# Kernel tuning notes

Measured on AMD Instinct MI355X. Metric: run time of the kernel, lower is better.

Reference implementation:

```python
import jax, jax.numpy as jnp
import numpy as np

N_NODES = 50000
N_EDGES = 800000
IN_DIM = 128
OUT_DIM = 128


def setup_inputs() -> dict:
    key = jax.random.key(0)
    k_h, k_w, k_src, k_dst = jax.random.split(key, 4)
    h = jax.random.normal(k_h, (N_NODES, IN_DIM), dtype=jnp.float32)
    # xavier-uniform weight
    limit = float(np.sqrt(6.0 / (IN_DIM + OUT_DIM)))
    W = jax.random.uniform(k_w, (IN_DIM, OUT_DIM), dtype=jnp.float32,
                           minval=-limit, maxval=limit)
    b = jnp.zeros((OUT_DIM,), dtype=jnp.float32)
    src = jax.random.randint(k_src, (N_EDGES,), 0, N_NODES, dtype=jnp.int64)
    dst = jax.random.randint(k_dst, (N_EDGES,), 0, N_NODES, dtype=jnp.int64)
    # GCN symmetric norm: deg^{-1/2} based on in-degree (clamped to >=1)
    deg = jax.ops.segment_sum(jnp.ones((N_EDGES,), jnp.float32), dst,
                              num_segments=N_NODES)
    norm = (jnp.maximum(deg, 1.0) ** -0.5)[:, None]  # [N,1]
    return {"h": h, "norm": norm, "W": W, "b": b, "src": src, "dst": dst}


def reference(h, norm, W, b, src, dst):
    # dense projection: [N, in] @ [in, out]
    h = h @ W
    # pre-aggregation norm scale
    h = h * norm
    # copy_src + sum: gather source features, segment-sum into destination nodes
    msgs = h[src]  # [E, out]
    h = jax.ops.segment_sum(msgs, dst, num_segments=h.shape[0])
    # post-aggregation norm scale + bias
    h = h * norm + b
    return h
```

## Files before the change

kernel.cpp:

```cpp
#include <hip/hip_runtime.h>

#define N_NODES 50000
#define N_EDGES 800000

#define NBUCKETS 391
#define BIN_EDGES 4096
#define BIN_NB 196
#define BUCKET_CAP 2560

#define GEMM_NB ((N_NODES + 63) / 64)
#define FUSED_NB 980

typedef __attribute__((ext_vector_type(4))) _Float16 half4;
typedef __attribute__((ext_vector_type(8))) _Float16 half8;
typedef __attribute__((ext_vector_type(4))) float f32x4;

__global__ __launch_bounds__(256) void prep_wt_kernel(
    const float* __restrict__ W, _Float16* __restrict__ Wt)
{
    const int e = blockIdx.x * 256 + threadIdx.x;
    const int c = e & 127;
    const int k4 = (e >> 7) << 2;
    half4 v;
    v.x = (_Float16)W[(k4 + 0) * 128 + c];
    v.y = (_Float16)W[(k4 + 1) * 128 + c];
    v.z = (_Float16)W[(k4 + 2) * 128 + c];
    v.w = (_Float16)W[(k4 + 3) * 128 + c];
    *(half4*)(Wt + (size_t)c * 128 + k4) = v;
}

__global__ __launch_bounds__(256) void fused_gemm_bin_kernel(
    const float* __restrict__ h, const float* __restrict__ norm,
    const _Float16* __restrict__ Wt, _Float16* __restrict__ t,
    const int* __restrict__ src, const int* __restrict__ dst,
    int* __restrict__ bcur, int* __restrict__ bucketbuf)
{
    __shared__ int hist[NBUCKETS];
    __shared__ __align__(16) _Float16 WtS[128 * 136];
    const int tid = threadIdx.x;
    const int bid = blockIdx.x;

    if (bid % 5 == 4) {
        const int bs = (bid / 5) * BIN_EDGES;
        for (int i = tid; i < NBUCKETS; i += 256) hist[i] = 0;
        __syncthreads();
#pragma unroll
        for (int j = 0; j < 4; ++j) {
            int e4 = bs + (j * 256 + tid) * 4;
            if (e4 < N_EDGES) {
                int4 d4 = *(const int4*)(dst + e4);
                atomicAdd(&hist[d4.x >> 7], 1);
                atomicAdd(&hist[d4.y >> 7], 1);
                atomicAdd(&hist[d4.z >> 7], 1);
                atomicAdd(&hist[d4.w >> 7], 1);
            }
        }
        __syncthreads();
        for (int i = tid; i < NBUCKETS; i += 256) {
            int hc = hist[i];
            hist[i] = hc ? atomicAdd(&bcur[i], hc) : 0;
        }
        __syncthreads();
#pragma unroll
        for (int j = 0; j < 4; ++j) {
            int e4 = bs + (j * 256 + tid) * 4;
            if (e4 < N_EDGES) {
                int4 d4 = *(const int4*)(dst + e4);
                int4 s4 = *(const int4*)(src + e4);
                int b0, p;
                b0 = d4.x >> 7; p = atomicAdd(&hist[b0], 1);
                bucketbuf[(size_t)b0 * BUCKET_CAP + p] = s4.x | ((d4.x & 127) << 16);
                b0 = d4.y >> 7; p = atomicAdd(&hist[b0], 1);
                bucketbuf[(size_t)b0 * BUCKET_CAP + p] = s4.y | ((d4.y & 127) << 16);
                b0 = d4.z >> 7; p = atomicAdd(&hist[b0], 1);
                bucketbuf[(size_t)b0 * BUCKET_CAP + p] = s4.z | ((d4.z & 127) << 16);
                b0 = d4.w >> 7; p = atomicAdd(&hist[b0], 1);
                bucketbuf[(size_t)b0 * BUCKET_CAP + p] = s4.w | ((d4.w & 127) << 16);
            }
        }
        return;
    }

    const int gemm_id = bid - bid / 5;
    if (gemm_id >= GEMM_NB) return;
    const int rbase = gemm_id * 64;

#pragma unroll
    for (int i = 0; i < 8; ++i) {
        int f = i * 256 + tid;
        int c = f >> 4;
        int k8 = (f & 15) << 3;
        *(half8*)(WtS + c * 136 + k8) = *(const half8*)(Wt + (size_t)c * 128 + k8);
    }
    __syncthreads();

    const int wid = tid >> 6, lane = tid & 63;
    const int lrow = lane & 15;
    const int khi = (lane >> 4) << 3;
    const int r0 = wid * 16;
    const int gr = rbase + r0 + lrow;

    half8 a[4];
#pragma unroll
    for (int ks = 0; ks < 4; ++ks) {
        float4 f0 = make_float4(0.f, 0.f, 0.f, 0.f);
        float4 f1 = f0;
        if (gr < N_NODES) {
            const float* hp = h + (size_t)gr * 128 + ks * 32 + khi;
            f0 = *(const float4*)hp;
            f1 = *(const float4*)(hp + 4);
        }
        half8 av;
        av[0] = (_Float16)f0.x; av[1] = (_Float16)f0.y;
        av[2] = (_Float16)f0.z; av[3] = (_Float16)f0.w;
        av[4] = (_Float16)f1.x; av[5] = (_Float16)f1.y;
        av[6] = (_Float16)f1.z; av[7] = (_Float16)f1.w;
        a[ks] = av;
    }

    const int rq = rbase + r0 + ((lane >> 4) << 2);
    float nv[4];
#pragma unroll
    for (int reg = 0; reg < 4; ++reg)
        nv[reg] = (rq + reg < N_NODES) ? norm[rq + reg] : 0.f;

#pragma unroll
    for (int ct = 0; ct < 8; ++ct) {
        const int c0 = ct * 16;
        f32x4 acc = {0.f, 0.f, 0.f, 0.f};
#pragma unroll
        for (int ks = 0; ks < 4; ++ks) {
            half8 bf = *(const half8*)(WtS + (c0 + lrow) * 136 + ks * 32 + khi);
            acc = __builtin_amdgcn_mfma_f32_16x16x32_f16(a[ks], bf, acc, 0, 0, 0);
        }
#pragma unroll
        for (int reg = 0; reg < 4; ++reg) {
            if (rq + reg < N_NODES)
                t[(size_t)(rq + reg) * 128 + c0 + lrow] = (_Float16)(acc[reg] * nv[reg]);
        }
    }
}

__global__ __launch_bounds__(256) void scatter_kernel(
    const int* __restrict__ bucketbuf, const int* __restrict__ bcur,
    int* __restrict__ off, int* __restrict__ cur, int* __restrict__ esrc)
{
    const int tid = threadIdx.x;
    const int b = blockIdx.x;
    __shared__ int hist[128];
    __shared__ int lcur[128];
    if (tid < 128) hist[tid] = 0;
    __syncthreads();

    const int n = bcur[b];
    const int* buf = bucketbuf + (size_t)b * BUCKET_CAP;
    for (int i = tid; i < n; i += 256)
        atomicAdd(&hist[(buf[i] >> 16) & 127], 1);
    __syncthreads();

    const int cnt = (tid < 128) ? hist[tid] : 0;
    for (int d = 1; d < 128; d <<= 1) {
        int v = 0;
        if (tid < 128 && tid >= d) v = hist[tid - d];
        __syncthreads();
        if (tid < 128) hist[tid] += v;
        __syncthreads();
    }
    const int base = b * BUCKET_CAP;
    int o0 = 0;
    if (tid < 128) {
        o0 = base + hist[tid] - cnt;
        lcur[tid] = o0;
    }
    __syncthreads();
    for (int i = tid; i < n; i += 256) {
        int p = buf[i];
        int pos = atomicAdd(&lcur[(p >> 16) & 127], 1);
        esrc[pos] = p & 0xFFFF;
    }
    __syncthreads();
    const int g = b * 128 + tid;
    if (tid < 128 && g < N_NODES) {
        off[g] = o0;
        cur[g] = lcur[tid];
    }
}

__global__ __launch_bounds__(256) void aggregate_kernel(
    const int* __restrict__ off, const int* __restrict__ cur,
    const int* __restrict__ esrc, const _Float16* __restrict__ t,
    const float* __restrict__ norm, const float* __restrict__ b,
    float* __restrict__ out)
{
    const int g = blockIdx.x * 16 + (threadIdx.x >> 4);
    if (g >= N_NODES) return;
    const int l = threadIdx.x & 15;
    const int c = l << 3;
    const int i0 = off[g], i1 = cur[g];

    float acc0[8], acc1[8], acc2[8], acc3[8];
#pragma unroll
    for (int j = 0; j < 8; ++j) {
        acc0[j] = 0.f; acc1[j] = 0.f; acc2[j] = 0.f; acc3[j] = 0.f;
    }

    int i = i0;
    for (; i + 4 <= i1; i += 4) {
        int s0 = esrc[i], s1 = esrc[i + 1], s2 = esrc[i + 2], s3 = esrc[i + 3];
        half8 v0 = *(const half8*)(t + (size_t)s0 * 128 + c);
        half8 v1 = *(const half8*)(t + (size_t)s1 * 128 + c);
        half8 v2 = *(const half8*)(t + (size_t)s2 * 128 + c);
        half8 v3 = *(const half8*)(t + (size_t)s3 * 128 + c);
#pragma unroll
        for (int j = 0; j < 8; ++j) {
            acc0[j] += (float)v0[j]; acc1[j] += (float)v1[j];
            acc2[j] += (float)v2[j]; acc3[j] += (float)v3[j];
        }
    }
    for (; i < i1; ++i) {
        int s0 = esrc[i];
        half8 v0 = *(const half8*)(t + (size_t)s0 * 128 + c);
#pragma unroll
        for (int j = 0; j < 8; ++j) acc0[j] += (float)v0[j];
    }

    const float nv = norm[g];
    const float4 b0 = *(const float4*)(b + c);
    const float4 b1 = *(const float4*)(b + c + 4);
    float4 o0 = make_float4((acc0[0] + acc1[0] + acc2[0] + acc3[0]) * nv + b0.x,
                            (acc0[1] + acc1[1] + acc2[1] + acc3[1]) * nv + b0.y,
                            (acc0[2] + acc1[2] + acc2[2] + acc3[2]) * nv + b0.z,
                            (acc0[3] + acc1[3] + acc2[3] + acc3[3]) * nv + b0.w);
    float4 o1 = make_float4((acc0[4] + acc1[4] + acc2[4] + acc3[4]) * nv + b1.x,
                            (acc0[5] + acc1[5] + acc2[5] + acc3[5]) * nv + b1.y,
                            (acc0[6] + acc1[6] + acc2[6] + acc3[6]) * nv + b1.z,
                            (acc0[7] + acc1[7] + acc2[7] + acc3[7]) * nv + b1.w);
    *(float4*)(out + (size_t)g * 128 + c) = o0;
    *(float4*)(out + (size_t)g * 128 + c + 4) = o1;
}

static inline size_t align256(size_t x) { return (x + 255) & ~(size_t)255; }

extern "C" void kernel_launch(void* const* d_in, const int* in_sizes, int n_in,
                              void* d_out, int out_size, void* d_ws, size_t ws_size,
                              hipStream_t stream)
{
    const float* h    = (const float*)d_in[0];
    const float* norm = (const float*)d_in[1];
    const float* W    = (const float*)d_in[2];
    const float* b    = (const float*)d_in[3];
    const int*   src  = (const int*)d_in[4];
    const int*   dst  = (const int*)d_in[5];
    float* out = (float*)d_out;

    char* ws = (char*)d_ws;
    size_t o = 0;
    _Float16* t = (_Float16*)(ws + o);  o = align256(o + (size_t)N_NODES * 128 * 2);
    _Float16* Wt = (_Float16*)(ws + o); o = align256(o + (size_t)128 * 128 * 2);
    int* off = (int*)(ws + o);          o = align256(o + (size_t)N_NODES * 4);
    int* cur = (int*)(ws + o);          o = align256(o + (size_t)N_NODES * 4);
    int* esrc = (int*)(ws + o);         o = align256(o + (size_t)NBUCKETS * BUCKET_CAP * 4);
    int* bcur = (int*)(ws + o);         o = align256(o + (size_t)NBUCKETS * 4);
    int* bucketbuf = (int*)(ws + o);    o = align256(o + (size_t)NBUCKETS * BUCKET_CAP * 4);

    hipMemsetAsync(bcur, 0, (size_t)NBUCKETS * 4, stream);
    prep_wt_kernel<<<16, 256, 0, stream>>>(W, Wt);
    fused_gemm_bin_kernel<<<FUSED_NB, 256, 0, stream>>>(h, norm, Wt, t,
                                                        src, dst, bcur, bucketbuf);
    scatter_kernel<<<NBUCKETS, 256, 0, stream>>>(bucketbuf, bcur, off, cur, esrc);
    aggregate_kernel<<<(N_NODES + 15) / 16, 256, 0, stream>>>(off, cur, esrc, t, norm, b, out);
}
```

Measured before the change: 72.58 us.

## Fuse bucket scatter with aggregation using shared-memory source lists

Merges the scatter and aggregate kernels into one. Each block sorts its bucket's edges by destination into a shared-memory list and then immediately gathers and sums source rows for its nodes. Buckets shrink from 128 to 64 nodes so the per-bucket source list fits in LDS, and the prefix scan becomes a wavefront shuffle scan. The bcur memset is folded into the weight prep kernel. This removes one launch and the global esrc/off/cur round trip, but aggregation now runs on only 782 blocks of 256 threads, each handling 4 nodes per 16-lane group in sequence, which may reduce parallelism. It also risks overflowing a 1280-entry bucket if edges are unevenly distributed.

```diff
diff --git a/kernel.cpp b/kernel.cpp
--- a/kernel.cpp
+++ b/kernel.cpp
@@ -3,10 +3,10 @@
 #define N_NODES 50000
 #define N_EDGES 800000
 
-#define NBUCKETS 391
+#define NBUCKETS 782
 #define BIN_EDGES 4096
 #define BIN_NB 196
-#define BUCKET_CAP 2560
+#define BUCKET_CAP 1280
 
 #define GEMM_NB ((N_NODES + 63) / 64)
 #define FUSED_NB 980
@@ -16,9 +16,14 @@
 typedef __attribute__((ext_vector_type(4))) float f32x4;
 
 __global__ __launch_bounds__(256) void prep_wt_kernel(
-    const float* __restrict__ W, _Float16* __restrict__ Wt)
-{
-    const int e = blockIdx.x * 256 + threadIdx.x;
+    const float* __restrict__ W, _Float16* __restrict__ Wt,
+    int* __restrict__ bcur)
+{
+    const int tid = threadIdx.x;
+    if (blockIdx.x == 0) {
+        for (int i = tid; i < NBUCKETS; i += 256) bcur[i] = 0;
+    }
+    const int e = blockIdx.x * 256 + tid;
     const int c = e & 127;
     const int k4 = (e >> 7) << 2;
     half4 v;
@@ -49,10 +54,10 @@
             int e4 = bs + (j * 256 + tid) * 4;
             if (e4 < N_EDGES) {
                 int4 d4 = *(const int4*)(dst + e4);
-                atomicAdd(&hist[d4.x >> 7], 1);
-                atomicAdd(&hist[d4.y >> 7], 1);
-                atomicAdd(&hist[d4.z >> 7], 1);
-                atomicAdd(&hist[d4.w >> 7], 1);
+                atomicAdd(&hist[d4.x >> 6], 1);
+                atomicAdd(&hist[d4.y >> 6], 1);
+                atomicAdd(&hist[d4.z >> 6], 1);
+                atomicAdd(&hist[d4.w >> 6], 1);
             }
         }
         __syncthreads();
@@ -68,14 +73,14 @@
                 int4 d4 = *(const int4*)(dst + e4);
                 int4 s4 = *(const int4*)(src + e4);
                 int b0, p;
-                b0 = d4.x >> 7; p = atomicAdd(&hist[b0], 1);
-                bucketbuf[(size_t)b0 * BUCKET_CAP + p] = s4.x | ((d4.x & 127) << 16);
-                b0 = d4.y >> 7; p = atomicAdd(&hist[b0], 1);
-                bucketbuf[(size_t)b0 * BUCKET_CAP + p] = s4.y | ((d4.y & 127) << 16);
-                b0 = d4.z >> 7; p = atomicAdd(&hist[b0], 1);
-                bucketbuf[(size_t)b0 * BUCKET_CAP + p] = s4.z | ((d4.z & 127) << 16);
-                b0 = d4.w >> 7; p = atomicAdd(&hist[b0], 1);
-                bucketbuf[(size_t)b0 * BUCKET_CAP + p] = s4.w | ((d4.w & 127) << 16);
+                b0 = d4.x >> 6; p = atomicAdd(&hist[b0], 1);
+                bucketbuf[(size_t)b0 * BUCKET_CAP + p] = s4.x | ((d4.x & 63) << 16);
+                b0 = d4.y >> 6; p = atomicAdd(&hist[b0], 1);
+                bucketbuf[(size_t)b0 * BUCKET_CAP + p] = s4.y | ((d4.y & 63) << 16);
+                b0 = d4.z >> 6; p = atomicAdd(&hist[b0], 1);
+                bucketbuf[(size_t)b0 * BUCKET_CAP + p] = s4.z | ((d4.z & 63) << 16);
+                b0 = d4.w >> 6; p = atomicAdd(&hist[b0], 1);
+                bucketbuf[(size_t)b0 * BUCKET_CAP + p] = s4.w | ((d4.w & 63) << 16);
             }
         }
         return;
@@ -141,102 +146,97 @@
     }
 }
 
-__global__ __launch_bounds__(256) void scatter_kernel(
+__global__ __launch_bounds__(256) void scatter_aggregate_kernel(
     const int* __restrict__ bucketbuf, const int* __restrict__ bcur,
-    int* __restrict__ off, int* __restrict__ cur, int* __restrict__ esrc)
+    const _Float16* __restrict__ t, const float* __restrict__ norm,
+    const float* __restrict__ bias, float* __restrict__ out)
 {
     const int tid = threadIdx.x;
     const int b = blockIdx.x;
-    __shared__ int hist[128];
-    __shared__ int lcur[128];
-    if (tid < 128) hist[tid] = 0;
+    __shared__ int cnt[64];
+    __shared__ int endp[64];
+    __shared__ int lcur[64];
+    __shared__ int slist[BUCKET_CAP];
+
+    if (tid < 64) cnt[tid] = 0;
     __syncthreads();
 
     const int n = bcur[b];
     const int* buf = bucketbuf + (size_t)b * BUCKET_CAP;
     for (int i = tid; i < n; i += 256)
-        atomicAdd(&hist[(buf[i] >> 16) & 127], 1);
-    __syncthreads();
-
-    const int cnt = (tid < 128) ? hist[tid] : 0;
-    for (int d = 1; d < 128; d <<= 1) {
-        int v = 0;
-        if (tid < 128 && tid >= d) v = hist[tid - d];
-        __syncthreads();
-        if (tid < 128) hist[tid] += v;
-        __syncthreads();
-    }
-    const int base = b * BUCKET_CAP;
-    int o0 = 0;
-    if (tid < 128) {
-        o0 = base + hist[tid] - cnt;
-        lcur[tid] = o0;
-    }
-    __syncthreads();
+        atomicAdd(&cnt[(buf[i] >> 16) & 63], 1);
+    __syncthreads();
+
+    if (tid < 64) {
+        int c = cnt[tid];
+        int inc = c;
+#pragma unroll
+        for (int d = 1; d < 64; d <<= 1) {
+            int u = __shfl_up(inc, d);
+            if (tid >= d) inc += u;
+        }
+        endp[tid] = inc;
+        lcur[tid] = inc - c;
+    }
+    __syncthreads();
+
     for (int i = tid; i < n; i += 256) {
         int p = buf[i];
-        int pos = atomicAdd(&lcur[(p >> 16) & 127], 1);
-        esrc[pos] = p & 0xFFFF;
-    }
-    __syncthreads();
-    const int g = b * 128 + tid;
-    if (tid < 128 && g < N_NODES) {
-        off[g] = o0;
-        cur[g] = lcur[tid];
-    }
-}
-
-__global__ __launch_bounds__(256) void aggregate_kernel(
-    const int* __restrict__ off, const int* __restrict__ cur,
-    const int* __restrict__ esrc, const _Float16* __restrict__ t,
-    const float* __restrict__ norm, const float* __restrict__ b,
-    float* __restrict__ out)
-{
-    const int g = blockIdx.x * 16 + (threadIdx.x >> 4);
-    if (g >= N_NODES) return;
-    const int l = threadIdx.x & 15;
-    const int c = l << 3;
-    const int i0 = off[g], i1 = cur[g];
-
-    float acc0[8], acc1[8], acc2[8], acc3[8];
-#pragma unroll
-    for (int j = 0; j < 8; ++j) {
-        acc0[j] = 0.f; acc1[j] = 0.f; acc2[j] = 0.f; acc3[j] = 0.f;
-    }
-
-    int i = i0;
-    for (; i + 4 <= i1; i += 4) {
-        int s0 = esrc[i], s1 = esrc[i + 1], s2 = esrc[i + 2], s3 = esrc[i + 3];
-        half8 v0 = *(const half8*)(t + (size_t)s0 * 128 + c);
-        half8 v1 = *(const half8*)(t + (size_t)s1 * 128 + c);
-        half8 v2 = *(const half8*)(t + (size_t)s2 * 128 + c);
-        half8 v3 = *(const half8*)(t + (size_t)s3 * 128 + c);
+        int pos = atomicAdd(&lcur[(p >> 16) & 63], 1);
+        slist[pos] = p & 0xFFFF;
+    }
+    __syncthreads();
+
+    const int q = tid >> 4, l = tid & 15, c = l << 3;
+    const float4 b0 = *(const float4*)(bias + c);
+    const float4 b1 = *(const float4*)(bias + c + 4);
+
+    for (int r = 0; r < 4; ++r) {
+        const int nl = q + (r << 4);
+        const int g = b * 64 + nl;
+        if (g >= N_NODES) continue;
+        const int i1 = endp[nl];
+        const int i0 = i1 - cnt[nl];
+
+        float acc0[8], acc1[8], acc2[8], acc3[8];
 #pragma unroll
         for (int j = 0; j < 8; ++j) {
-            acc0[j] += (float)v0[j]; acc1[j] += (float)v1[j];
-            acc2[j] += (float)v2[j]; acc3[j] += (float)v3[j];
-        }
-    }
-    for (; i < i1; ++i) {
-        int s0 = esrc[i];
-        half8 v0 = *(const half8*)(t + (size_t)s0 * 128 + c);
-#pragma unroll
-        for (int j = 0; j < 8; ++j) acc0[j] += (float)v0[j];
-    }
-
-    const float nv = norm[g];
-    const float4 b0 = *(const float4*)(b + c);
-    const float4 b1 = *(const float4*)(b + c + 4);
-    float4 o0 = make_float4((acc0[0] + acc1[0] + acc2[0] + acc3[0]) * nv + b0.x,
-                            (acc0[1] + acc1[1] + acc2[1] + acc3[1]) * nv + b0.y,
-                            (acc0[2] + acc1[2] + acc2[2] + acc3[2]) * nv + b0.z,
-                            (acc0[3] + acc1[3] + acc2[3] + acc3[3]) * nv + b0.w);
-    float4 o1 = make_float4((acc0[4] + acc1[4] + acc2[4] + acc3[4]) * nv + b1.x,
-                            (acc0[5] + acc1[5] + acc2[5] + acc3[5]) * nv + b1.y,
-                            (acc0[6] + acc1[6] + acc2[6] + acc3[6]) * nv + b1.z,
-                            (acc0[7] + acc1[7] + acc2[7] + acc3[7]) * nv + b1.w);
-    *(float4*)(out + (size_t)g * 128 + c) = o0;
-    *(float4*)(out + (size_t)g * 128 + c + 4) = o1;
+            acc0[j] = 0.f; acc1[j] = 0.f; acc2[j] = 0.f; acc3[j] = 0.f;
+        }
+
+        int i = i0;
+        for (; i + 4 <= i1; i += 4) {
+            int s0 = slist[i], s1 = slist[i + 1];
+            int s2 = slist[i + 2], s3 = slist[i + 3];
+            half8 v0 = *(const half8*)(t + (size_t)s0 * 128 + c);
+            half8 v1 = *(const half8*)(t + (size_t)s1 * 128 + c);
+            half8 v2 = *(const half8*)(t + (size_t)s2 * 128 + c);
+            half8 v3 = *(const half8*)(t + (size_t)s3 * 128 + c);
+#pragma unroll
+            for (int j = 0; j < 8; ++j) {
+                acc0[j] += (float)v0[j]; acc1[j] += (float)v1[j];
+                acc2[j] += (float)v2[j]; acc3[j] += (float)v3[j];
+            }
+        }
+        for (; i < i1; ++i) {
+            int s0 = slist[i];
+            half8 v0 = *(const half8*)(t + (size_t)s0 * 128 + c);
+#pragma unroll
+            for (int j = 0; j < 8; ++j) acc0[j] += (float)v0[j];
+        }
+
+        const float nv = norm[g];
+        float4 o0 = make_float4((acc0[0] + acc1[0] + acc2[0] + acc3[0]) * nv + b0.x,
+                                (acc0[1] + acc1[1] + acc2[1] + acc3[1]) * nv + b0.y,
+                                (acc0[2] + acc1[2] + acc2[2] + acc3[2]) * nv + b0.z,
+                                (acc0[3] + acc1[3] + acc2[3] + acc3[3]) * nv + b0.w);
+        float4 o1 = make_float4((acc0[4] + acc1[4] + acc2[4] + acc3[4]) * nv + b1.x,
+                                (acc0[5] + acc1[5] + acc2[5] + acc3[5]) * nv + b1.y,
+                                (acc0[6] + acc1[6] + acc2[6] + acc3[6]) * nv + b1.z,
+                                (acc0[7] + acc1[7] + acc2[7] + acc3[7]) * nv + b1.w);
+        *(float4*)(out + (size_t)g * 128 + c) = o0;
+        *(float4*)(out + (size_t)g * 128 + c + 4) = o1;
+    }
 }
 
 static inline size_t align256(size_t x) { return (x + 255) & ~(size_t)255; }
@@ -257,16 +257,12 @@
     size_t o = 0;
     _Float16* t = (_Float16*)(ws + o);  o = align256(o + (size_t)N_NODES * 128 * 2);
     _Float16* Wt = (_Float16*)(ws + o); o = align256(o + (size_t)128 * 128 * 2);
-    int* off = (int*)(ws + o);          o = align256(o + (size_t)N_NODES * 4);
-    int* cur = (int*)(ws + o);          o = align256(o + (size_t)N_NODES * 4);
-    int* esrc = (int*)(ws + o);         o = align256(o + (size_t)NBUCKETS * BUCKET_CAP * 4);
     int* bcur = (int*)(ws + o);         o = align256(o + (size_t)NBUCKETS * 4);
     int* bucketbuf = (int*)(ws + o);    o = align256(o + (size_t)NBUCKETS * BUCKET_CAP * 4);
 
-    hipMemsetAsync(bcur, 0, (size_t)NBUCKETS * 4, stream);
-    prep_wt_kernel<<<16, 256, 0, stream>>>(W, Wt);
+    prep_wt_kernel<<<16, 256, 0, stream>>>(W, Wt, bcur);
     fused_gemm_bin_kernel<<<FUSED_NB, 256, 0, stream>>>(h, norm, Wt, t,
                                                         src, dst, bcur, bucketbuf);
-    scatter_kernel<<<NBUCKETS, 256, 0, stream>>>(bucketbuf, bcur, off, cur, esrc);
-    aggregate_kernel<<<(N_NODES + 15) / 16, 256, 0, stream>>>(off, cur, esrc, t, norm, b, out);
-}
+    scatter_aggregate_kernel<<<NBUCKETS, 256, 0, stream>>>(bucketbuf, bcur,
+                                                           t, norm, b, out);
+}
```

After: 60.13 us. -17.2%, faster.
